# Performance work log

Measured on AMD Instinct MI355X. Metric: run time of the kernel, lower is better.

The kernel has to match this reference:

```python
import jax, jax.numpy as jnp
import numpy as np
import math

NUM_HEADS = 16
SPARSITY_RATIO = 0.1
MASK_KEY_SEED = 42


def _sparse_mask(seq_length):
    """Band (+/-2 around diagonal) OR random num_random columns per row. [S,S] float32 of {0,1}."""
    i = jnp.arange(seq_length)
    band = (jnp.abs(i[:, None] - i[None, :]) <= 2).astype(jnp.float32)
    num_random = max(1, int(seq_length * SPARSITY_RATIO))
    u = jax.random.uniform(jax.random.key(MASK_KEY_SEED), (seq_length, seq_length))
    _, idx = jax.lax.top_k(u, num_random)  # [S, num_random] random distinct cols per row
    rand_mask = jnp.zeros((seq_length, seq_length), jnp.float32).at[i[:, None], idx].set(1.0)
    return jnp.maximum(band, rand_mask)


def setup_inputs() -> dict:
    key = jax.random.key(0)
    ks = jax.random.split(key, 7)
    B, S, H = 2, 2048, 1024
    scale = 0.02
    return {
        "hidden_states": jax.random.normal(ks[0], (B, S, H), jnp.float32),
        "Wq": jax.random.normal(ks[1], (H, H), jnp.float32) * scale,
        "bq": jnp.zeros((H,), jnp.float32),
        "Wk": jax.random.normal(ks[2], (H, H), jnp.float32) * scale,
        "bk": jnp.zeros((H,), jnp.float32),
        "Wv": jax.random.normal(ks[3], (H, H), jnp.float32) * scale,
        "bv": jnp.zeros((H,), jnp.float32),
    }


def reference(hidden_states, Wq, bq, Wk, bk, Wv, bv):
    B, S, H = hidden_states.shape
    nh = NUM_HEADS
    hd = H // nh

    def proj(W, b):
        # nn.Linear: x @ W.T + b, then [B,S,nh,hd] -> [B,nh,S,hd]
        y = jnp.einsum('bsh,oh->bso', hidden_states, W) + b
        return y.reshape(B, S, nh, hd).transpose(0, 2, 1, 3)

    q = proj(Wq, bq)
    k = proj(Wk, bk)
    v = proj(Wv, bv)

    scores = jnp.einsum('bhqd,bhkd->bhqk', q, k) / math.sqrt(hd)
    mask = _sparse_mask(S)  # [S,S], broadcast over batch and heads
    scores = scores * mask  # multiplicative mask (masked scores become 0, NOT -inf)
    probs = jax.nn.softmax(scores, axis=-1)
    ctx = jnp.einsum('bhqk,bhkd->bhqd', probs, v)
    return ctx.transpose(0, 2, 1, 3).reshape(B, S, H)
```

## Files before the change

kernel.cpp:

```cpp
#include <hip/hip_runtime.h>


typedef unsigned int u32;
typedef unsigned short u16;
typedef float f32x4 __attribute__((ext_vector_type(4)));
typedef short s16x8 __attribute__((ext_vector_type(8)));
typedef u32  u32x4 __attribute__((ext_vector_type(4)));
typedef u16  u16x4 __attribute__((ext_vector_type(4)));

__device__ __forceinline__ u16 f2bf(float f) {
  u32 u = __builtin_bit_cast(u32, f);
  return (u16)((u + 0x7FFFu + ((u >> 16) & 1u)) >> 16);
}

__device__ __forceinline__ void async16(void* lds, const void* g) {
  __builtin_amdgcn_global_load_lds((const __attribute__((address_space(1))) u32*)g,
                                   (__attribute__((address_space(3))) u32*)lds, 16, 0, 0);
}

__global__ __launch_bounds__(256) void cast_kernel(const float* __restrict__ src,
                                                   u16* __restrict__ dst, int n4) {
  int i = blockIdx.x * 256 + threadIdx.x;
  if (i < n4) {
    float4 v = ((const float4*)src)[i];
    u16x4 o = { f2bf(v.x), f2bf(v.y), f2bf(v.z), f2bf(v.w) };
    ((u16x4*)dst)[i] = o;
  }
}

__device__ __forceinline__ void threefry(u32 x0, u32 x1, u32& y0, u32& y1) {
  const u32 k0 = 0u, k1 = 42u, k2 = 0u ^ 42u ^ 0x1BD11BDAu;
  x0 += k0; x1 += k1;
#define TFR(r) { x0 += x1; x1 = (x1 << r) | (x1 >> (32 - r)); x1 ^= x0; }
  TFR(13) TFR(15) TFR(26) TFR(6)  x0 += k1; x1 += k2 + 1u;
  TFR(17) TFR(29) TFR(16) TFR(24) x0 += k2; x1 += k0 + 2u;
  TFR(13) TFR(15) TFR(26) TFR(6)  x0 += k0; x1 += k1 + 3u;
  TFR(17) TFR(29) TFR(16) TFR(24) x0 += k1; x1 += k2 + 4u;
  TFR(13) TFR(15) TFR(26) TFR(6)  x0 += k2; x1 += k0 + 5u;
#undef TFR
  y0 = x0; y1 = x1;
}

#define NRAND 204

__global__ __launch_bounds__(256) void mask_kernel(u32* __restrict__ maskbits) {
  __shared__ u32 hist[256];
  __shared__ u32 mwords[64];
  __shared__ u32 candV[128];
  __shared__ u32 candC[128];
  __shared__ u32 used[128];
  __shared__ u32 scal[4];

  const int tid = threadIdx.x;
  const int row = blockIdx.x;
  hist[tid] = 0;
  if (tid < 64) mwords[tid] = 0;
  if (tid < 128) used[tid] = 0;
  if (tid == 0) scal[2] = 0;
  __syncthreads();

  u32 k23[8];
#pragma unroll
  for (int j = 0; j < 8; ++j) {
    u32 c = (u32)tid * 8u + (u32)j;
    u32 flat = (u32)row * 2048u + c;
    u32 y0, y1; threefry(0u, flat, y0, y1);
    u32 bits = y0 ^ y1;
    k23[j] = bits >> 9;
    atomicAdd(&hist[k23[j] >> 15], 1u);
  }
  __syncthreads();
  for (int off = 1; off < 256; off <<= 1) {
    u32 add = (tid + off < 256) ? hist[tid + off] : 0u;
    __syncthreads();
    hist[tid] += add;
    __syncthreads();
  }
  u32 Sv = hist[tid];
  u32 Sn = (tid < 255) ? hist[tid + 1] : 0u;
  if (Sv >= NRAND && Sn < NRAND) { scal[0] = (u32)tid; scal[1] = NRAND - Sn; }
  __syncthreads();
  const u32 bin = scal[0];
  const u32 need = scal[1];
#pragma unroll
  for (int j = 0; j < 8; ++j) {
    if ((k23[j] >> 15) == bin) {
      u32 p = atomicAdd(&scal[2], 1u);
      if (p < 128u) { candV[p] = k23[j]; candC[p] = (u32)tid * 8u + (u32)j; }
    }
  }
  __syncthreads();
  if (tid == 0) {
    int n = (int)(scal[2] < 128u ? scal[2] : 128u);
    for (u32 t = 0; t < need; ++t) {
      int best = -1;
      for (int i2 = 0; i2 < n; ++i2) {
        if (used[i2]) continue;
        if (best < 0 || candV[i2] > candV[best] ||
            (candV[i2] == candV[best] && candC[i2] < candC[best])) best = i2;
      }
      if (best < 0) break;
      used[best] = 1;
      atomicOr(&mwords[candC[best] >> 5], 1u << (candC[best] & 31u));
    }
  }
#pragma unroll
  for (int j = 0; j < 8; ++j) {
    u32 c = (u32)tid * 8u + (u32)j;
    if ((k23[j] >> 15) > bin) atomicOr(&mwords[c >> 5], 1u << (c & 31u));
  }
  if (tid < 5) {
    int c = row - 2 + tid;
    if (c >= 0 && c < 2048) atomicOr(&mwords[c >> 5], 1u << (c & 31u));
  }
  __syncthreads();
  if (tid < 64) maskbits[row * 64 + tid] = mwords[tid];
}

__global__ __launch_bounds__(256) void gemm_qkv(
    const u16* __restrict__ Xbf, const u16* __restrict__ Wbf3,
    const float* __restrict__ bq, const float* __restrict__ bk,
    const float* __restrict__ bv,
    u16* __restrict__ Qbf, u16* __restrict__ Kbf, u16* __restrict__ VtB) {
  __shared__ u16 smem[128 * 136];
  u16* As = smem;
  u16* Bs = smem + 4096;

  const int tid  = threadIdx.x;
  const int lane = tid & 63;
  const int w    = tid >> 6;
  const int wr = w >> 1, wc = w & 1;
  const int l15 = lane & 15, l4 = lane >> 4;
  const int mBase = blockIdx.x * 128;
  const int nBase = blockIdx.y * 128;
  const int z = blockIdx.z;
  const u16* Bmat = Wbf3 + z * 1048576;
  const float* bias = (z == 0) ? bq : (z == 1) ? bk : bv;

  const int ci1 = tid, ci2 = tid + 256;
  const int r1 = ci1 >> 2, c1 = ci1 & 3, cc1 = c1 ^ ((r1 >> 1) & 3);
  const int r2 = ci2 >> 2, c2 = ci2 & 3, cc2 = c2 ^ ((r2 >> 1) & 3);

  f32x4 acc[4][4];
#pragma unroll
  for (int i = 0; i < 4; ++i)
#pragma unroll
    for (int j = 0; j < 4; ++j) acc[i][j] = {0.f, 0.f, 0.f, 0.f};

  for (int k0 = 0; k0 < 1024; k0 += 32) {
    async16(As + ci1 * 8, Xbf + (mBase + r1) * 1024 + k0 + cc1 * 8);
    async16(As + ci2 * 8, Xbf + (mBase + r2) * 1024 + k0 + cc2 * 8);
    async16(Bs + ci1 * 8, Bmat + (nBase + r1) * 1024 + k0 + cc1 * 8);
    async16(Bs + ci2 * 8, Bmat + (nBase + r2) * 1024 + k0 + cc2 * 8);
    __syncthreads();
    s16x8 a[4], b[4];
#pragma unroll
    for (int f = 0; f < 4; ++f) {
      int rl = wr * 64 + f * 16 + l15;
      a[f] = *(const s16x8*)(As + rl * 32 + ((l4 ^ ((rl >> 1) & 3)) * 8));
    }
#pragma unroll
    for (int f = 0; f < 4; ++f) {
      int rl = wc * 64 + f * 16 + l15;
      b[f] = *(const s16x8*)(Bs + rl * 32 + ((l4 ^ ((rl >> 1) & 3)) * 8));
    }
#pragma unroll
    for (int i = 0; i < 4; ++i)
#pragma unroll
      for (int j = 0; j < 4; ++j)
        acc[i][j] = __builtin_amdgcn_mfma_f32_16x16x32_bf16(a[i], b[j], acc[i][j], 0, 0, 0);
    __syncthreads();
  }

  const float scale = (z == 0) ? 0.125f : 1.0f;
  if (z < 2) {
    u16* dst = (z == 0) ? Qbf : Kbf;
#pragma unroll
    for (int i = 0; i < 4; ++i)
#pragma unroll
      for (int j = 0; j < 4; ++j) {
        int ng = nBase + wc * 64 + j * 16 + l15;
        int h = ng >> 6, d = ng & 63;
        float bb = bias[ng];
#pragma unroll
        for (int r = 0; r < 4; ++r) {
          int mg = mBase + wr * 64 + i * 16 + l4 * 4 + r;
          int bbi = mg >> 11, s = mg & 2047;
          dst[(((bbi * 16 + h) * 2048 + s) * 64) + d] = f2bf((acc[i][j][r] + bb) * scale);
        }
      }
  } else {
    u16* ct = smem;
#pragma unroll
    for (int i = 0; i < 4; ++i)
#pragma unroll
      for (int j = 0; j < 4; ++j) {
        int nl = wc * 64 + j * 16 + l15;
        int ml = wr * 64 + i * 16 + l4 * 4;
        float bb = bias[nBase + nl];
        u16x4 p = { f2bf(acc[i][j][0] + bb), f2bf(acc[i][j][1] + bb),
                    f2bf(acc[i][j][2] + bb), f2bf(acc[i][j][3] + bb) };
        *(u16x4*)(ct + nl * 136 + ml) = p;
      }
    __syncthreads();
#pragma unroll
    for (int it = 0; it < 8; ++it) {
      int ci = tid + it * 256;
      int nl = ci >> 4, m8 = ci & 15;
      int ng = nBase + nl, mg = mBase + m8 * 8;
      int h = ng >> 6, d = ng & 63;
      int bbi = mg >> 11, s = mg & 2047;
      s16x8 v = *(const s16x8*)(ct + nl * 136 + m8 * 8);
      *(s16x8*)(VtB + (((bbi * 16 + h) * 64 + d) * 2048) + s) = v;
    }
  }
}

__global__ __launch_bounds__(256) void attn_kernel(
    const u16* __restrict__ Qbf, const u16* __restrict__ Kbf,
    const u16* __restrict__ Vt, const u32* __restrict__ maskbits,
    float* __restrict__ out) {
  __shared__ u16 KbS[64 * 64];
  __shared__ u16 VtS[64 * 64];
  __shared__ u32 maskT[64 * 68];
  __shared__ u16 Pls[4][16 * 72];

  const int tid  = threadIdx.x;
  const int lane = tid & 63;
  const int w    = tid >> 6;
  const int l15 = lane & 15, l4 = lane >> 4;
  const int qt = blockIdx.x;
  const int bh = blockIdx.y;
  const int qbase = qt * 64;

  for (int idx = tid; idx < 4096; idx += 256) {
    int ww = idx & 63, qr = idx >> 6;
    maskT[ww * 68 + qr] = maskbits[(qbase + qr) * 64 + ww];
  }

  const int qrow = qbase + w * 16 + l15;
  const u16* qp = Qbf + ((bh * 2048 + qrow) * 64) + l4 * 8;
  s16x8 qa0 = *(const s16x8*)(qp);
  s16x8 qa1 = *(const s16x8*)(qp + 32);

  const f32x4 fzero = {0.f, 0.f, 0.f, 0.f};
  f32x4 acc[4];
#pragma unroll
  for (int d = 0; d < 4; ++d) acc[d] = fzero;
  float rs[4] = {0.f, 0.f, 0.f, 0.f};

  const int rkA = tid >> 3, cA = tid & 7, csA = cA ^ (rkA & 7);
  const int ci2 = tid + 256;
  const int rkB = ci2 >> 3, cB = ci2 & 7, csB = cB ^ (rkB & 7);

  for (int kt = 0; kt < 32; ++kt) {
    const int kb = kt * 64;
    async16(KbS + tid * 8, Kbf + ((bh * 2048 + kb + rkA) * 64) + csA * 8);
    async16(VtS + tid * 8, Vt + ((bh * 64 + rkA) * 2048) + kb + csA * 8);
    async16(KbS + ci2 * 8, Kbf + ((bh * 2048 + kb + rkB) * 64) + csB * 8);
    async16(VtS + ci2 * 8, Vt + ((bh * 64 + rkB) * 2048) + kb + csB * 8);
    __syncthreads();

    f32x4 sc[4];
#pragma unroll
    for (int fn = 0; fn < 4; ++fn) {
      int key = fn * 16 + l15;
      s16x8 kf0 = *(const s16x8*)(KbS + key * 64 + ((l4 ^ (key & 7)) * 8));
      s16x8 kf1 = *(const s16x8*)(KbS + key * 64 + (((l4 + 4) ^ (key & 7)) * 8));
      sc[fn] = __builtin_amdgcn_mfma_f32_16x16x32_bf16(qa0, kf0, fzero, 0, 0, 0);
      sc[fn] = __builtin_amdgcn_mfma_f32_16x16x32_bf16(qa1, kf1, sc[fn], 0, 0, 0);
    }

#pragma unroll
    for (int fn = 0; fn < 4; ++fn) {
      int wi = kt * 2 + (fn >> 1);
      u32x4 mw = *(const u32x4*)(maskT + wi * 68 + w * 16 + l4 * 4);
      u32 bp = (u32)((fn & 1) * 16 + l15);
#pragma unroll
      for (int r = 0; r < 4; ++r) {
        float sv = ((mw[r] >> bp) & 1u) ? sc[fn][r] : 0.0f;
        float p = __expf(sv);
        rs[r] += p;
        Pls[w][(l4 * 4 + r) * 72 + fn * 16 + l15] = f2bf(p);
      }
    }

    s16x8 pa0 = *(const s16x8*)(Pls[w] + l15 * 72 + l4 * 8);
    s16x8 pa1 = *(const s16x8*)(Pls[w] + l15 * 72 + l4 * 8 + 32);
#pragma unroll
    for (int df = 0; df < 4; ++df) {
      int dl = df * 16 + l15;
      s16x8 vf0 = *(const s16x8*)(VtS + dl * 64 + ((l4 ^ (dl & 7)) * 8));
      s16x8 vf1 = *(const s16x8*)(VtS + dl * 64 + (((l4 + 4) ^ (dl & 7)) * 8));
      acc[df] = __builtin_amdgcn_mfma_f32_16x16x32_bf16(pa0, vf0, acc[df], 0, 0, 0);
      acc[df] = __builtin_amdgcn_mfma_f32_16x16x32_bf16(pa1, vf1, acc[df], 0, 0, 0);
    }
    __syncthreads();
  }

#pragma unroll
  for (int r = 0; r < 4; ++r) {
    float v = rs[r];
    v += __shfl_xor(v, 1); v += __shfl_xor(v, 2);
    v += __shfl_xor(v, 4); v += __shfl_xor(v, 8);
    rs[r] = 1.0f / v;
  }
  const int b = bh >> 4, h = bh & 15;
#pragma unroll
  for (int df = 0; df < 4; ++df) {
    int col = h * 64 + df * 16 + l15;
#pragma unroll
    for (int r = 0; r < 4; ++r) {
      int qg = qbase + w * 16 + l4 * 4 + r;
      out[(b * 2048 + qg) * 1024 + col] = acc[df][r] * rs[r];
    }
  }
}

extern "C" void kernel_launch(void* const* d_in, const int* in_sizes, int n_in,
                              void* d_out, int out_size, void* d_ws, size_t ws_size,
                              hipStream_t stream) {
  const float* hs = (const float*)d_in[0];
  const float* Wq = (const float*)d_in[1];
  const float* bq = (const float*)d_in[2];
  const float* Wk = (const float*)d_in[3];
  const float* bk = (const float*)d_in[4];
  const float* Wv = (const float*)d_in[5];
  const float* bv = (const float*)d_in[6];
  float* out = (float*)d_out;
  char* ws = (char*)d_ws;

  u32* maskbits = (u32*)(ws);
  u16* Xbf  = (u16*)(ws + 524288);
  u16* Wbf3 = (u16*)(ws + 524288 + 8388608);
  u16* Qbf  = (u16*)(ws + 15204352);
  u16* Kbf  = (u16*)(ws + 23592960);
  u16* Vt   = (u16*)(ws + 31981568);

  cast_kernel<<<4096, 256, 0, stream>>>(hs, Xbf, 1048576);
  cast_kernel<<<1024, 256, 0, stream>>>(Wq, Wbf3,           262144);
  cast_kernel<<<1024, 256, 0, stream>>>(Wk, Wbf3 + 1048576, 262144);
  cast_kernel<<<1024, 256, 0, stream>>>(Wv, Wbf3 + 2097152, 262144);
  mask_kernel<<<2048, 256, 0, stream>>>(maskbits);
  gemm_qkv<<<dim3(32, 8, 3), 256, 0, stream>>>(Xbf, Wbf3, bq, bk, bv, Qbf, Kbf, Vt);
  attn_kernel<<<dim3(32, 32), 256, 0, stream>>>(Qbf, Kbf, Vt, maskbits, out);
}
```

Measured before the change: 252.9 us.

## Double-buffer K tiles, load V and mask straight into registers, permute Vt layout

The attention loop now double-buffers the K tile in LDS and prefetches the next tile while the current one is computed. V fragments and mask words are read straight from global memory into registers, which drops the V LDS tile and the transposed mask staging. The projection epilogue permutes key order inside each 64-key block of Vt, so the packed P layout in LDS matches it and P can be written as 4-wide vectors. The change also adds an XCD-aware block remap and a launch-bounds occupancy hint of 4, at the cost of more per-thread global loads and register pressure.

Result: slower. 310.2 us (+22.7%).

```diff
diff --git a/kernel.cpp b/kernel.cpp
--- a/kernel.cpp
+++ b/kernel.cpp
@@ -5,6 +5,7 @@
 typedef unsigned short u16;
 typedef float f32x4 __attribute__((ext_vector_type(4)));
 typedef short s16x8 __attribute__((ext_vector_type(8)));
+typedef u16  u16x8 __attribute__((ext_vector_type(8)));
 typedef u32  u32x4 __attribute__((ext_vector_type(4)));
 typedef u16  u16x4 __attribute__((ext_vector_type(4)));
 
@@ -196,11 +197,11 @@
 #pragma unroll
       for (int j = 0; j < 4; ++j) {
         int nl = wc * 64 + j * 16 + l15;
-        int ml = wr * 64 + i * 16 + l4 * 4;
         float bb = bias[nBase + nl];
-        u16x4 p = { f2bf(acc[i][j][0] + bb), f2bf(acc[i][j][1] + bb),
-                    f2bf(acc[i][j][2] + bb), f2bf(acc[i][j][3] + bb) };
-        *(u16x4*)(ct + nl * 136 + ml) = p;
+        int base = nl * 136 + wr * 64 + 16 * l4 + i;
+#pragma unroll
+        for (int r = 0; r < 4; ++r)
+          ct[base + 4 * r] = f2bf(acc[i][j][r] + bb);
       }
     __syncthreads();
 #pragma unroll
@@ -216,33 +217,39 @@
   }
 }
 
-__global__ __launch_bounds__(256) void attn_kernel(
+__global__ __launch_bounds__(256, 4) void attn_kernel(
     const u16* __restrict__ Qbf, const u16* __restrict__ Kbf,
     const u16* __restrict__ Vt, const u32* __restrict__ maskbits,
     float* __restrict__ out) {
-  __shared__ u16 KbS[64 * 64];
-  __shared__ u16 VtS[64 * 64];
-  __shared__ u32 maskT[64 * 68];
-  __shared__ u16 Pls[4][16 * 72];
+  __shared__ u16 Kb[2][4096];
+  __shared__ u16 Pls[4][1152];
 
   const int tid  = threadIdx.x;
   const int lane = tid & 63;
   const int w    = tid >> 6;
   const int l15 = lane & 15, l4 = lane >> 4;
-  const int qt = blockIdx.x;
-  const int bh = blockIdx.y;
+
+  const int lin = blockIdx.x + 32 * blockIdx.y;
+  const int wg  = (lin & 7) * 128 + (lin >> 3);
+  const int qt = wg & 31;
+  const int bh = wg >> 5;
   const int qbase = qt * 64;
-
-  for (int idx = tid; idx < 4096; idx += 256) {
-    int ww = idx & 63, qr = idx >> 6;
-    maskT[ww * 68 + qr] = maskbits[(qbase + qr) * 64 + ww];
-  }
 
   const int qrow = qbase + w * 16 + l15;
   const u16* qp = Qbf + ((bh * 2048 + qrow) * 64) + l4 * 8;
   s16x8 qa0 = *(const s16x8*)(qp);
   s16x8 qa1 = *(const s16x8*)(qp + 32);
 
+  const u32* mrow[4];
+#pragma unroll
+  for (int r = 0; r < 4; ++r)
+    mrow[r] = maskbits + (qbase + w * 16 + l4 * 4 + r) * 64;
+
+  const u16* vrow[4];
+#pragma unroll
+  for (int df = 0; df < 4; ++df)
+    vrow[df] = Vt + (size_t)(bh * 64 + df * 16 + l15) * 2048;
+
   const f32x4 fzero = {0.f, 0.f, 0.f, 0.f};
   f32x4 acc[4];
 #pragma unroll
@@ -252,49 +259,74 @@
   const int rkA = tid >> 3, cA = tid & 7, csA = cA ^ (rkA & 7);
   const int ci2 = tid + 256;
   const int rkB = ci2 >> 3, cB = ci2 & 7, csB = cB ^ (rkB & 7);
+  const u16* kgbase = Kbf + (size_t)(bh * 2048) * 64;
+
+  async16(Kb[0] + tid * 8, kgbase + rkA * 64 + csA * 8);
+  async16(Kb[0] + ci2 * 8, kgbase + rkB * 64 + csB * 8);
+  asm volatile("s_waitcnt vmcnt(0)" ::: "memory");
+  __syncthreads();
+
+  u16* Pw = Pls[w];
 
   for (int kt = 0; kt < 32; ++kt) {
     const int kb = kt * 64;
-    async16(KbS + tid * 8, Kbf + ((bh * 2048 + kb + rkA) * 64) + csA * 8);
-    async16(VtS + tid * 8, Vt + ((bh * 64 + rkA) * 2048) + kb + csA * 8);
-    async16(KbS + ci2 * 8, Kbf + ((bh * 2048 + kb + rkB) * 64) + csB * 8);
-    async16(VtS + ci2 * 8, Vt + ((bh * 64 + rkB) * 2048) + kb + csB * 8);
-    __syncthreads();
+    const int cur = kt & 1;
+
+    s16x8 vf0[4], vf1[4];
+#pragma unroll
+    for (int df = 0; df < 4; ++df) {
+      vf0[df] = *(const s16x8*)(vrow[df] + kb + l4 * 8);
+      vf1[df] = *(const s16x8*)(vrow[df] + kb + 32 + l4 * 8);
+    }
+    uint2 mw2[4];
+#pragma unroll
+    for (int r = 0; r < 4; ++r)
+      mw2[r] = *(const uint2*)(mrow[r] + kt * 2);
+
+    if (kt < 31) {
+      const u16* kg = kgbase + (kb + 64) * 64;
+      async16(Kb[cur ^ 1] + tid * 8, kg + rkA * 64 + csA * 8);
+      async16(Kb[cur ^ 1] + ci2 * 8, kg + rkB * 64 + csB * 8);
+    }
 
     f32x4 sc[4];
 #pragma unroll
     for (int fn = 0; fn < 4; ++fn) {
       int key = fn * 16 + l15;
-      s16x8 kf0 = *(const s16x8*)(KbS + key * 64 + ((l4 ^ (key & 7)) * 8));
-      s16x8 kf1 = *(const s16x8*)(KbS + key * 64 + (((l4 + 4) ^ (key & 7)) * 8));
+      s16x8 kf0 = *(const s16x8*)(Kb[cur] + key * 64 + ((l4 ^ (key & 7)) * 8));
+      s16x8 kf1 = *(const s16x8*)(Kb[cur] + key * 64 + (((l4 + 4) ^ (key & 7)) * 8));
       sc[fn] = __builtin_amdgcn_mfma_f32_16x16x32_bf16(qa0, kf0, fzero, 0, 0, 0);
       sc[fn] = __builtin_amdgcn_mfma_f32_16x16x32_bf16(qa1, kf1, sc[fn], 0, 0, 0);
     }
 
 #pragma unroll
-    for (int fn = 0; fn < 4; ++fn) {
-      int wi = kt * 2 + (fn >> 1);
-      u32x4 mw = *(const u32x4*)(maskT + wi * 68 + w * 16 + l4 * 4);
-      u32 bp = (u32)((fn & 1) * 16 + l15);
-#pragma unroll
-      for (int r = 0; r < 4; ++r) {
-        float sv = ((mw[r] >> bp) & 1u) ? sc[fn][r] : 0.0f;
-        float p = __expf(sv);
-        rs[r] += p;
-        Pls[w][(l4 * 4 + r) * 72 + fn * 16 + l15] = f2bf(p);
+    for (int r = 0; r < 4; ++r) {
+      float p[4];
+#pragma unroll
+      for (int fn = 0; fn < 4; ++fn) {
+        u32 word = (fn < 2) ? mw2[r].x : mw2[r].y;
+        u32 bp = (u32)((fn & 1) * 16 + l15);
+        float sv = ((word >> bp) & 1u) ? sc[fn][r] : 0.0f;
+        p[fn] = __expf(sv);
       }
-    }
-
-    s16x8 pa0 = *(const s16x8*)(Pls[w] + l15 * 72 + l4 * 8);
-    s16x8 pa1 = *(const s16x8*)(Pls[w] + l15 * 72 + l4 * 8 + 32);
+      rs[r] += (p[0] + p[1]) + (p[2] + p[3]);
+      u16x4 pk = { f2bf(p[0]), f2bf(p[1]), f2bf(p[2]), f2bf(p[3]) };
+      *(u16x4*)(Pw + (l4 * 4 + r) * 72 + l15 * 4) = pk;
+    }
+
+    __builtin_amdgcn_sched_barrier(0);
+
+    u16x8 t0 = *(const u16x8*)(Pw + l15 * 72 + l4 * 8);
+    u16x8 t1 = *(const u16x8*)(Pw + l15 * 72 + 32 + l4 * 8);
+    s16x8 pa0 = __builtin_bit_cast(s16x8, t0);
+    s16x8 pa1 = __builtin_bit_cast(s16x8, t1);
 #pragma unroll
     for (int df = 0; df < 4; ++df) {
-      int dl = df * 16 + l15;
-      s16x8 vf0 = *(const s16x8*)(VtS + dl * 64 + ((l4 ^ (dl & 7)) * 8));
-      s16x8 vf1 = *(const s16x8*)(VtS + dl * 64 + (((l4 + 4) ^ (dl & 7)) * 8));
-      acc[df] = __builtin_amdgcn_mfma_f32_16x16x32_bf16(pa0, vf0, acc[df], 0, 0, 0);
-      acc[df] = __builtin_amdgcn_mfma_f32_16x16x32_bf16(pa1, vf1, acc[df], 0, 0, 0);
-    }
+      acc[df] = __builtin_amdgcn_mfma_f32_16x16x32_bf16(pa0, vf0[df], acc[df], 0, 0, 0);
+      acc[df] = __builtin_amdgcn_mfma_f32_16x16x32_bf16(pa1, vf1[df], acc[df], 0, 0, 0);
+    }
+
+    asm volatile("s_waitcnt vmcnt(0)" ::: "memory");
     __syncthreads();
   }
 
```
